# Performance work log

Hardware: AMD Instinct MI355X
Metric: run time of the kernel (lower is better)

The kernel has to match this reference:

```python
import jax, jax.numpy as jnp
import numpy as np

L, B, D, H, E, K, R = 256, 64, 1024, 16, 8, 2, 64
SCALE_ADAPTER = 0.1


def setup_inputs() -> dict:
    key = jax.random.key(0)
    ks = jax.random.split(key, 10)
    rn = lambda k, shape, s=0.02: jax.random.normal(k, shape, jnp.float32) * s
    return {
        "x": jax.random.normal(ks[0], (L, B, D), jnp.float32),
        "ln1_w": jnp.ones((D,), jnp.float32), "ln1_b": jnp.zeros((D,), jnp.float32),
        "in_proj_w": rn(ks[1], (3 * D, D)), "in_proj_b": jnp.zeros((3 * D,), jnp.float32),
        "out_proj_w": rn(ks[2], (D, D)), "out_proj_b": jnp.zeros((D,), jnp.float32),
        "ln2_w": jnp.ones((D,), jnp.float32), "ln2_b": jnp.zeros((D,), jnp.float32),
        "c_fc_w": rn(ks[3], (4 * D, D)), "c_fc_b": jnp.zeros((4 * D,), jnp.float32),
        "c_proj_w": rn(ks[4], (D, 4 * D)), "c_proj_b": jnp.zeros((D,), jnp.float32),
        "w_gate": rn(ks[5], (D, E), 0.05),
        "down_w": rn(ks[6], (E, R, D)), "down_b": jnp.zeros((E, R), jnp.float32),
        "up_w": rn(ks[7], (E, D, R)), "up_b": jnp.zeros((E, D), jnp.float32),
    }


def _layer_norm(x, w, b, eps=1e-5):
    mu = x.mean(-1, keepdims=True)
    var = ((x - mu) ** 2).mean(-1, keepdims=True)
    return (x - mu) / jnp.sqrt(var + eps) * w + b


def _mha(x, in_w, in_b, out_w, out_b):
    # x: (L,B,D) sequence-first, self-attention q=k=v=x
    hd = D // H
    qkv = x @ in_w.T + in_b                       # (L,B,3D)
    q, k, v = jnp.split(qkv, 3, axis=-1)
    q = q.reshape(L, B, H, hd)
    k = k.reshape(L, B, H, hd)
    v = v.reshape(L, B, H, hd)
    scores = jnp.einsum("lbhd,mbhd->bhlm", q, k) / jnp.sqrt(jnp.float32(hd))
    attn = jax.nn.softmax(scores, axis=-1)
    o = jnp.einsum("bhlm,mbhd->lbhd", attn, v).reshape(L, B, D)
    return o @ out_w.T + out_b


def _cv_squared(t):
    t = t.astype(jnp.float32)
    return t.var(ddof=1) / (t.mean() ** 2 + 1e-10)


def reference(x, ln1_w, ln1_b, in_proj_w, in_proj_b, out_proj_w, out_proj_b,
              ln2_w, ln2_b, c_fc_w, c_fc_b, c_proj_w, c_proj_b,
              w_gate, down_w, down_b, up_w, up_b):
    x = x + _mha(_layer_norm(x, ln1_w, ln1_b), in_proj_w, in_proj_b, out_proj_w, out_proj_b)

    # --- noisy top-k gating (eval path: no noise), routed on token 0 per sequence ---
    logits = x[0] @ w_gate                                    # (B,E)
    top_v, top_i = jax.lax.top_k(logits, min(K + 1, E))
    gk = jax.nn.softmax(top_v[:, :K], axis=1)                 # (B,K)
    gates = jnp.zeros((B, E), jnp.float32).at[jnp.arange(B)[:, None], top_i[:, :K]].set(gk)
    importance = gates.sum(0)
    load = (gates > 0).sum(0)
    moe_loss = (_cv_squared(importance) + _cv_squared(load)) * 0.01

    # --- dense dispatch/combine: y[l,b] = sum_e gates[b,e] * adapter_e(x[l,b]) ---
    h = jax.nn.relu(jnp.einsum("lbd,erd->lber", x, down_w) + down_b)     # (L,B,E,R)
    y = jnp.einsum("lber,edr,be->lbd", h, up_w, gates) + (gates @ up_b)[None]
    y = y * SCALE_ADAPTER

    # --- MLP (QuickGELU) + parallel adapter residual ---
    h2 = _layer_norm(x, ln2_w, ln2_b) @ c_fc_w.T + c_fc_b
    h2 = h2 * jax.nn.sigmoid(1.702 * h2)
    mlp = h2 @ c_proj_w.T + c_proj_b
    x = x + mlp + y
    return x, moe_loss
```

## Files before the change

kernel.cpp:

```cpp
#include <hip/hip_runtime.h>

typedef unsigned short u16;
typedef unsigned int u32;
typedef __bf16 bf16x8 __attribute__((ext_vector_type(8)));
typedef float f32x4 __attribute__((ext_vector_type(4)));

#define MFMA16(a, b, c) __builtin_amdgcn_mfma_f32_16x16x32_bf16(a, b, c, 0, 0, 0)

__device__ __forceinline__ u16 f2bf(float f) {
  u32 u = __builtin_bit_cast(u32, f);
  u32 r = u + 0x7fffu + ((u >> 16) & 1u);
  return (u16)(r >> 16);
}

__device__ __forceinline__ uint4 cvt8(const float4& a, const float4& b) {
  union { u16 h[8]; uint4 q; } u;
  u.h[0] = f2bf(a.x); u.h[1] = f2bf(a.y); u.h[2] = f2bf(a.z); u.h[3] = f2bf(a.w);
  u.h[4] = f2bf(b.x); u.h[5] = f2bf(b.y); u.h[6] = f2bf(b.z); u.h[7] = f2bf(b.w);
  return u.q;
}

__device__ __forceinline__ void gload16(const u16* g, u16* l) {
  __builtin_amdgcn_global_load_lds(
      (const __attribute__((address_space(1))) u32*)g,
      (__attribute__((address_space(3))) u32*)l, 16, 0, 0);
}

template <int MODE, int ASRC>
__global__ __launch_bounds__(256) void gemm_k(
    const void* __restrict__ Av, int lda,
    const u16* __restrict__ W, int ldb,
    const float* __restrict__ bias, const float* __restrict__ aux0,
    float* __restrict__ outF, u16* __restrict__ outB, int N, int K)
{
  __shared__ u16 As[128 * 32];
  __shared__ u16 Bs[128 * 32];
  const int tid = threadIdx.x;
  const int nxb = gridDim.x >> 7;
  const int gsz = nxb << 5;
  const int g = blockIdx.x / gsz;
  const int rem = blockIdx.x - g * gsz;
  const int m0 = ((g << 5) + (rem & 31)) * 128;
  const int n0 = (rem >> 5) * 128;
  const int w = tid >> 6, lane = tid & 63, lr = lane & 15, quad = lane >> 4;
  const int wm = (w >> 1) * 64, wn = (w & 1) * 64;

  f32x4 acc[4][4];
  #pragma unroll
  for (int i = 0; i < 4; i++)
    #pragma unroll
    for (int j = 0; j < 4; j++)
      #pragma unroll
      for (int r = 0; r < 4; r++) acc[i][j][r] = 0.f;

  const int srow = w * 32 + (lane >> 2);
  const int scol = (lane & 3) * 8;
  const u16* gB0 = W + (long)(n0 + srow) * ldb + scol;
  const u16* gB1 = gB0 + (long)16 * ldb;
  u16* lB0 = Bs + w * 1024;
  u16* lB1 = lB0 + 512;

  const u16* gA0 = nullptr; const u16* gA1 = nullptr;
  u16* lA0 = As + w * 1024; u16* lA1 = lA0 + 512;
  const float* F1 = nullptr; const float* F2 = nullptr;
  const int r0 = tid >> 2, ch0 = (tid & 3) * 8;
  if constexpr (ASRC == 0) {
    gA0 = (const u16*)Av + (long)(m0 + srow) * lda + scol;
    gA1 = gA0 + (long)16 * lda;
  } else {
    F1 = (const float*)Av + (long)(m0 + r0) * lda + ch0;
    F2 = (const float*)Av + (long)(m0 + r0 + 64) * lda + ch0;
  }

  for (int k0 = 0; k0 < K; k0 += 32) {
    if constexpr (ASRC == 0) {
      gload16(gA0 + k0, lA0);
      gload16(gA1 + k0, lA1);
      gload16(gB0 + k0, lB0);
      gload16(gB1 + k0, lB1);
      __syncthreads();
    } else {
      float4 p0 = *(const float4*)(F1 + k0);
      float4 p1 = *(const float4*)(F1 + k0 + 4);
      float4 q0 = *(const float4*)(F2 + k0);
      float4 q1 = *(const float4*)(F2 + k0 + 4);
      __syncthreads();
      gload16(gB0 + k0, lB0);
      gload16(gB1 + k0, lB1);
      *(uint4*)&As[r0 * 32 + ch0] = cvt8(p0, p1);
      *(uint4*)&As[(r0 + 64) * 32 + ch0] = cvt8(q0, q1);
      __syncthreads();
    }
    bf16x8 bfr[4];
    #pragma unroll
    for (int j = 0; j < 4; j++)
      bfr[j] = *(const bf16x8*)&Bs[(wn + j * 16 + lr) * 32 + quad * 8];
    #pragma unroll
    for (int i = 0; i < 4; i++) {
      bf16x8 af = *(const bf16x8*)&As[(wm + i * 16 + lr) * 32 + quad * 8];
      #pragma unroll
      for (int j = 0; j < 4; j++)
        acc[i][j] = MFMA16(af, bfr[j], acc[i][j]);
    }
    __syncthreads();
  }

  #pragma unroll
  for (int i = 0; i < 4; i++) {
    #pragma unroll
    for (int j = 0; j < 4; j++) {
      #pragma unroll
      for (int r = 0; r < 4; r++) {
        const int gm = m0 + wm + i * 16 + quad * 4 + r;
        const int gn = n0 + wn + j * 16 + lr;
        const long oidx = (long)gm * N + gn;
        float v = acc[i][j][r];
        if constexpr (MODE == 0) {
          v += bias[gn];
          outB[oidx] = f2bf(v);
        } else if constexpr (MODE == 1) {
          v += bias[gn] + aux0[oidx];
          outF[oidx] = v;
        } else if constexpr (MODE == 2) {
          v += bias[gn];
          v = fmaxf(v, 0.f);
          float g2 = aux0[(gm & 63) * 8 + (gn >> 6)];
          outB[oidx] = f2bf(v * g2);
        } else if constexpr (MODE == 3) {
          outF[oidx] += 0.1f * (v + aux0[(gm & 63) * 1024 + gn]);
        } else if constexpr (MODE == 4) {
          v += bias[gn];
          float e = __expf(-1.702f * v);
          v = v * __builtin_amdgcn_rcpf(1.f + e);
          outB[oidx] = f2bf(v);
        } else {
          if (bias) v += bias[gn];
          outF[oidx] += v;
        }
      }
    }
  }
}

__global__ __launch_bounds__(256) void attn_k(u16* __restrict__ qkv)
{
  __shared__ u16 Vt[64 * 264];
  __shared__ u16 Ps[32 * 264];
  __shared__ float rowstat[64];
  float* red = (float*)Ps;
  const int bh = blockIdx.x, b = bh >> 4, h = bh & 15;
  const int tid = threadIdx.x, w = tid >> 6, lane = tid & 63;
  const int lr = lane & 15, quad = lane >> 4;
  const long base = (long)b * 3072 + h * 64;

  for (int c = tid; c < 2048; c += 256) {
    int m = c >> 3, ch = (c & 7) * 8;
    uint4 vv = *(const uint4*)(qkv + (long)m * 196608 + base + 2048 + ch);
    const u16* s = (const u16*)&vv;
    #pragma unroll
    for (int t = 0; t < 8; t++) Vt[(ch + t) * 264 + m] = s[t];
  }
  __syncthreads();

  for (int qb = 0; qb < 4; qb++) {
    f32x4 acc[4][4];
    #pragma unroll
    for (int i = 0; i < 4; i++)
      #pragma unroll
      for (int j = 0; j < 4; j++)
        #pragma unroll
        for (int r = 0; r < 4; r++) acc[i][j][r] = 0.f;

    #pragma unroll
    for (int ks = 0; ks < 2; ks++) {
      bf16x8 bfr[4];
      #pragma unroll
      for (int j = 0; j < 4; j++) {
        int key = w * 64 + j * 16 + lr;
        bfr[j] = *(const bf16x8*)(qkv + (long)key * 196608 + base + 1024 + ks * 32 + quad * 8);
      }
      #pragma unroll
      for (int i = 0; i < 4; i++) {
        int gq = qb * 64 + i * 16 + lr;
        bf16x8 af = *(const bf16x8*)(qkv + (long)gq * 196608 + base + ks * 32 + quad * 8);
        #pragma unroll
        for (int j = 0; j < 4; j++)
          acc[i][j] = MFMA16(af, bfr[j], acc[i][j]);
      }
    }

    #pragma unroll
    for (int i = 0; i < 4; i++) {
      #pragma unroll
      for (int r = 0; r < 4; r++) {
        float m = -1e30f;
        #pragma unroll
        for (int j = 0; j < 4; j++) {
          float s = acc[i][j][r] * 0.125f;
          acc[i][j][r] = s;
          m = fmaxf(m, s);
        }
        #pragma unroll
        for (int off = 1; off < 16; off <<= 1) m = fmaxf(m, __shfl_xor(m, off));
        if (lr == 0) red[w * 64 + i * 16 + quad * 4 + r] = m;
      }
    }
    __syncthreads();
    if (tid < 64)
      rowstat[tid] = fmaxf(fmaxf(red[tid], red[64 + tid]),
                           fmaxf(red[128 + tid], red[192 + tid]));
    __syncthreads();

    #pragma unroll
    for (int i = 0; i < 4; i++) {
      #pragma unroll
      for (int r = 0; r < 4; r++) {
        float rm = rowstat[i * 16 + quad * 4 + r];
        float s = 0.f;
        #pragma unroll
        for (int j = 0; j < 4; j++) {
          float e = __expf(acc[i][j][r] - rm);
          acc[i][j][r] = e;
          s += e;
        }
        #pragma unroll
        for (int off = 1; off < 16; off <<= 1) s += __shfl_xor(s, off);
        if (lr == 0) red[w * 64 + i * 16 + quad * 4 + r] = s;
      }
    }
    __syncthreads();
    if (tid < 64)
      rowstat[tid] = red[tid] + red[64 + tid] + red[128 + tid] + red[192 + tid];
    __syncthreads();

    #pragma unroll
    for (int hf = 0; hf < 2; hf++) {
      #pragma unroll
      for (int ii = 0; ii < 2; ii++) {
        int i = hf * 2 + ii;
        #pragma unroll
        for (int r = 0; r < 4; r++) {
          int row = i * 16 + quad * 4 + r;
          float inv = 1.f / rowstat[row];
          #pragma unroll
          for (int j = 0; j < 4; j++)
            Ps[(row - hf * 32) * 264 + w * 64 + j * 16 + lr] =
                f2bf(acc[i][j][r] * inv);
        }
      }
      __syncthreads();
      f32x4 o[2];
      #pragma unroll
      for (int j2 = 0; j2 < 2; j2++)
        #pragma unroll
        for (int r = 0; r < 4; r++) o[j2][r] = 0.f;
      #pragma unroll
      for (int ks = 0; ks < 8; ks++) {
        bf16x8 af = *(const bf16x8*)&Ps[((w >> 1) * 16 + lr) * 264 + ks * 32 + quad * 8];
        #pragma unroll
        for (int j2 = 0; j2 < 2; j2++) {
          int j = (w & 1) * 2 + j2;
          bf16x8 bv = *(const bf16x8*)&Vt[(j * 16 + lr) * 264 + ks * 32 + quad * 8];
          o[j2] = MFMA16(af, bv, o[j2]);
        }
      }
      int l0 = qb * 64 + hf * 32 + (w >> 1) * 16 + quad * 4;
      #pragma unroll
      for (int j2 = 0; j2 < 2; j2++) {
        int j = (w & 1) * 2 + j2;
        #pragma unroll
        for (int r = 0; r < 4; r++)
          qkv[(long)(l0 + r) * 196608 + base + j * 16 + lr] = f2bf(o[j2][r]);
      }
      __syncthreads();
    }
  }
}

__global__ __launch_bounds__(256) void ln_k(const float* __restrict__ x,
                                            const float* __restrict__ wt,
                                            const float* __restrict__ bs,
                                            u16* __restrict__ out)
{
  const int tok = blockIdx.x * 4 + (threadIdx.x >> 6);
  const int lane = threadIdx.x & 63;
  const float* xp = x + (long)tok * 1024;
  float4 v[4];
  float s = 0.f, s2 = 0.f;
  #pragma unroll
  for (int t = 0; t < 4; t++) {
    v[t] = *(const float4*)(xp + t * 256 + lane * 4);
    s += v[t].x + v[t].y + v[t].z + v[t].w;
    s2 += v[t].x * v[t].x + v[t].y * v[t].y + v[t].z * v[t].z + v[t].w * v[t].w;
  }
  #pragma unroll
  for (int off = 32; off >= 1; off >>= 1) {
    s += __shfl_xor(s, off);
    s2 += __shfl_xor(s2, off);
  }
  const float m = s * (1.f / 1024.f);
  const float rstd = rsqrtf(s2 * (1.f / 1024.f) - m * m + 1e-5f);
  u16* op = out + (long)tok * 1024;
  #pragma unroll
  for (int t = 0; t < 4; t++) {
    int d = t * 256 + lane * 4;
    float4 wv = *(const float4*)(wt + d);
    float4 bv = *(const float4*)(bs + d);
    union { u16 h[4]; uint2 q; } o;
    o.h[0] = f2bf((v[t].x - m) * rstd * wv.x + bv.x);
    o.h[1] = f2bf((v[t].y - m) * rstd * wv.y + bv.y);
    o.h[2] = f2bf((v[t].z - m) * rstd * wv.z + bv.z);
    o.h[3] = f2bf((v[t].w - m) * rstd * wv.w + bv.w);
    *(uint2*)(op + d) = o.q;
  }
}

__global__ void cvtk(const float* __restrict__ src, u16* __restrict__ dst, int n4)
{
  int i = blockIdx.x * 256 + threadIdx.x;
  if (i >= n4) return;
  float4 v = ((const float4*)src)[i];
  union { u16 h[4]; uint2 q; } o;
  o.h[0] = f2bf(v.x); o.h[1] = f2bf(v.y); o.h[2] = f2bf(v.z); o.h[3] = f2bf(v.w);
  ((uint2*)dst)[i] = o.q;
}

__global__ void wupk(const float* __restrict__ up_w, u16* __restrict__ dst)
{
  int i = blockIdx.x * 256 + threadIdx.x;
  int r = i & 63, e = (i >> 6) & 7, d = i >> 9;
  dst[i] = f2bf(up_w[(e * 1024 + d) * 64 + r]);
}

__global__ __launch_bounds__(256) void gate_k(const float* __restrict__ x1,
                                              const float* __restrict__ wg,
                                              float* __restrict__ gates)
{
  const int wv = threadIdx.x >> 6, lane = threadIdx.x & 63;
  const int b = blockIdx.x * 4 + wv;
  const float* xp = x1 + (long)b * 1024;
  float lg[8];
  #pragma unroll
  for (int e = 0; e < 8; e++) lg[e] = 0.f;
  for (int i = 0; i < 16; i++) {
    int d = i * 64 + lane;
    float xv = xp[d];
    #pragma unroll
    for (int e = 0; e < 8; e++) lg[e] += xv * wg[d * 8 + e];
  }
  #pragma unroll
  for (int e = 0; e < 8; e++)
    #pragma unroll
    for (int off = 32; off >= 1; off >>= 1) lg[e] += __shfl_xor(lg[e], off);
  if (lane == 0) {
    int e1 = 0; float v1 = lg[0];
    #pragma unroll
    for (int e = 1; e < 8; e++) if (lg[e] > v1) { v1 = lg[e]; e1 = e; }
    int e2 = -1; float v2 = -1e30f;
    #pragma unroll
    for (int e = 0; e < 8; e++) if (e != e1 && lg[e] > v2) { v2 = lg[e]; e2 = e; }
    float ex = __expf(v2 - v1);
    float inv = 1.f / (1.f + ex);
    #pragma unroll
    for (int e = 0; e < 8; e++)
      gates[b * 8 + e] = (e == e1) ? inv : ((e == e2) ? ex * inv : 0.f);
  }
}

__global__ void moe_loss_k(const float* __restrict__ gates, float* __restrict__ out)
{
  if (threadIdx.x != 0) return;
  float imp[8], ld[8];
  for (int e = 0; e < 8; e++) { imp[e] = 0.f; ld[e] = 0.f; }
  for (int b = 0; b < 64; b++)
    for (int e = 0; e < 8; e++) {
      float g = gates[b * 8 + e];
      imp[e] += g;
      if (g > 0.f) ld[e] += 1.f;
    }
  float mi = 0.f, ml = 0.f;
  for (int e = 0; e < 8; e++) { mi += imp[e]; ml += ld[e]; }
  mi *= 0.125f; ml *= 0.125f;
  float vi = 0.f, vl = 0.f;
  for (int e = 0; e < 8; e++) {
    float a = imp[e] - mi; vi += a * a;
    float c = ld[e] - ml; vl += c * c;
  }
  vi *= (1.f / 7.f); vl *= (1.f / 7.f);
  out[0] = 0.01f * (vi / (mi * mi + 1e-10f) + vl / (ml * ml + 1e-10f));
}

__global__ __launch_bounds__(256) void gb_k(const float* __restrict__ gates,
                                            const float* __restrict__ up_b,
                                            float* __restrict__ gb)
{
  int b = blockIdx.x, d0 = threadIdx.x * 4;
  float g[8];
  #pragma unroll
  for (int e = 0; e < 8; e++) g[e] = gates[b * 8 + e];
  float s0 = 0, s1 = 0, s2 = 0, s3 = 0;
  #pragma unroll
  for (int e = 0; e < 8; e++) {
    float4 u = *(const float4*)(up_b + e * 1024 + d0);
    s0 += g[e] * u.x; s1 += g[e] * u.y; s2 += g[e] * u.z; s3 += g[e] * u.w;
  }
  float4 r; r.x = s0; r.y = s1; r.z = s2; r.w = s3;
  *(float4*)(gb + b * 1024 + d0) = r;
}

extern "C" void kernel_launch(void* const* d_in, const int* in_sizes, int n_in,
                              void* d_out, int out_size, void* d_ws, size_t ws_size,
                              hipStream_t stream)
{
  (void)in_sizes; (void)n_in; (void)out_size;
  const float* x      = (const float*)d_in[0];
  const float* ln1_w  = (const float*)d_in[1];
  const float* ln1_b  = (const float*)d_in[2];
  const float* in_w   = (const float*)d_in[3];
  const float* in_b   = (const float*)d_in[4];
  const float* out_w  = (const float*)d_in[5];
  const float* out_b  = (const float*)d_in[6];
  const float* ln2_w  = (const float*)d_in[7];
  const float* ln2_b  = (const float*)d_in[8];
  const float* fc_w   = (const float*)d_in[9];
  const float* fc_b   = (const float*)d_in[10];
  const float* pj_w   = (const float*)d_in[11];
  const float* pj_b   = (const float*)d_in[12];
  const float* w_gate = (const float*)d_in[13];
  const float* down_w = (const float*)d_in[14];
  const float* down_b = (const float*)d_in[15];
  const float* up_w   = (const float*)d_in[16];
  const float* up_b   = (const float*)d_in[17];
  float* out = (float*)d_out;
  char* ws = (char*)d_ws;

  u16* wb_in   = (u16*)(ws + 0);
  u16* wb_out  = (u16*)(ws + 6291456);
  u16* wb_down = (u16*)(ws + 8388608);
  u16* wb_up   = (u16*)(ws + 9437184);
  u16* wb_fc   = (u16*)(ws + 0);
  u16* wb_pj   = (u16*)(ws + 10485760);
  float* gates = (float*)(ws + 19005440);
  float* gb    = (float*)(ws + 19007488);
  u16* qkv     = (u16*)(ws + 19269632);
  u16* xln2    = (u16*)(ws + 19269632);
  u16* hg      = (u16*)(ws + 52824064);
  u16* h2      = (u16*)(ws + 69601280);
  u16* xln = (u16*)d_out;

  const bool big = ws_size >= (size_t)203819008;

  cvtk<<<3072, 256, 0, stream>>>(in_w, wb_in, 786432);
  cvtk<<<1024, 256, 0, stream>>>(out_w, wb_out, 262144);
  cvtk<<<512, 256, 0, stream>>>(down_w, wb_down, 131072);
  wupk<<<2048, 256, 0, stream>>>(up_w, wb_up);

  ln_k<<<4096, 256, 0, stream>>>(x, ln1_w, ln1_b, xln);
  gemm_k<0, 0><<<24 * 128, 256, 0, stream>>>(
      xln, 1024, wb_in, 1024, in_b, nullptr, nullptr, qkv, 3072, 1024);

  attn_k<<<1024, 256, 0, stream>>>(qkv);

  gemm_k<1, 0><<<8 * 128, 256, 0, stream>>>(
      qkv, 3072, wb_out, 1024, out_b, x, out, nullptr, 1024, 1024);

  gate_k<<<16, 256, 0, stream>>>(out, w_gate, gates);
  moe_loss_k<<<1, 64, 0, stream>>>(gates, out + 16777216);
  gb_k<<<64, 256, 0, stream>>>(gates, up_b, gb);

  ln_k<<<4096, 256, 0, stream>>>(out, ln2_w, ln2_b, xln2);

  gemm_k<2, 2><<<4 * 128, 256, 0, stream>>>(
      out, 1024, wb_down, 1024, down_b, gates, nullptr, hg, 512, 1024);
  gemm_k<3, 0><<<8 * 128, 256, 0, stream>>>(
      hg, 512, wb_up, 512, nullptr, gb, out, nullptr, 1024, 512);

  cvtk<<<4096, 256, 0, stream>>>(fc_w, wb_fc, 1048576);
  cvtk<<<4096, 256, 0, stream>>>(pj_w, wb_pj, 1048576);

  if (big) {
    gemm_k<4, 0><<<32 * 128, 256, 0, stream>>>(
        xln2, 1024, wb_fc, 1024, fc_b, nullptr, nullptr, h2, 4096, 1024);
    gemm_k<5, 0><<<8 * 128, 256, 0, stream>>>(
        h2, 4096, wb_pj, 4096, pj_b, nullptr, out, nullptr, 1024, 4096);
  } else {
    for (int c = 0; c < 4; c++) {
      gemm_k<4, 0><<<8 * 128, 256, 0, stream>>>(
          xln2, 1024, wb_fc + (long)c * 1048576, 1024, fc_b + c * 1024,
          nullptr, nullptr, h2, 1024, 1024);
      gemm_k<5, 0><<<8 * 128, 256, 0, stream>>>(
          h2, 1024, wb_pj + c * 1024, 4096, (c == 0) ? pj_b : nullptr,
          nullptr, out, nullptr, 1024, 1024);
    }
  }
}
```

Baseline: 1.082 ms.

## Double-buffer GEMM shared-memory tiles to overlap global loads with MFMA

Splits the A and B LDS tiles into two buffers. The kernel prefetches the next K-slice into the idle buffer while MFMAs consume the current one, which drops one barrier per iteration. For fp32 A inputs, the next slice is loaded into registers before the MFMAs and converted and stored to LDS after them. This doubles LDS use per block, which may lower occupancy, and adds register pressure from the held prefetch values. The fp32 store path is guarded only for ASRC==2, so any other non-zero ASRC would never write its A tile.

```diff
diff --git a/kernel.cpp b/kernel.cpp
--- a/kernel.cpp
+++ b/kernel.cpp
@@ -33,8 +33,8 @@
     const float* __restrict__ bias, const float* __restrict__ aux0,
     float* __restrict__ outF, u16* __restrict__ outB, int N, int K)
 {
-  __shared__ u16 As[128 * 32];
-  __shared__ u16 Bs[128 * 32];
+  __shared__ u16 As[2][128 * 32];
+  __shared__ u16 Bs[2][128 * 32];
   const int tid = threadIdx.x;
   const int nxb = gridDim.x >> 7;
   const int gsz = nxb << 5;
@@ -57,11 +57,9 @@
   const int scol = (lane & 3) * 8;
   const u16* gB0 = W + (long)(n0 + srow) * ldb + scol;
   const u16* gB1 = gB0 + (long)16 * ldb;
-  u16* lB0 = Bs + w * 1024;
-  u16* lB1 = lB0 + 512;
+  const int lo = w * 1024;
 
   const u16* gA0 = nullptr; const u16* gA1 = nullptr;
-  u16* lA0 = As + w * 1024; u16* lA1 = lA0 + 512;
   const float* F1 = nullptr; const float* F2 = nullptr;
   const int r0 = tid >> 2, ch0 = (tid & 3) * 8;
   if constexpr (ASRC == 0) {
@@ -72,37 +70,71 @@
     F2 = (const float*)Av + (long)(m0 + r0 + 64) * lda + ch0;
   }
 
+  int cur = 0;
+
+  if constexpr (ASRC == 0) {
+    gload16(gA0, &As[0][lo]);
+    gload16(gA1, &As[0][lo + 512]);
+    gload16(gB0, &Bs[0][lo]);
+    gload16(gB1, &Bs[0][lo + 512]);
+  } else {
+    float4 p0 = *(const float4*)(F1);
+    float4 p1 = *(const float4*)(F1 + 4);
+    float4 q0 = *(const float4*)(F2);
+    float4 q1 = *(const float4*)(F2 + 4);
+    gload16(gB0, &Bs[0][lo]);
+    gload16(gB1, &Bs[0][lo + 512]);
+    *(uint4*)&As[0][r0 * 32 + ch0] = cvt8(p0, p1);
+    *(uint4*)&As[0][(r0 + 64) * 32 + ch0] = cvt8(q0, q1);
+  }
+  __syncthreads();
+
   for (int k0 = 0; k0 < K; k0 += 32) {
+    const int kn = k0 + 32;
+    const bool more = kn < K;
+
+    float4 p0, p1, q0, q1;
     if constexpr (ASRC == 0) {
-      gload16(gA0 + k0, lA0);
-      gload16(gA1 + k0, lA1);
-      gload16(gB0 + k0, lB0);
-      gload16(gB1 + k0, lB1);
-      __syncthreads();
+      if (more) {
+        gload16(gA0 + kn, &As[cur ^ 1][lo]);
+        gload16(gA1 + kn, &As[cur ^ 1][lo + 512]);
+        gload16(gB0 + kn, &Bs[cur ^ 1][lo]);
+        gload16(gB1 + kn, &Bs[cur ^ 1][lo + 512]);
+      }
     } else {
-      float4 p0 = *(const float4*)(F1 + k0);
-      float4 p1 = *(const float4*)(F1 + k0 + 4);
-      float4 q0 = *(const float4*)(F2 + k0);
-      float4 q1 = *(const float4*)(F2 + k0 + 4);
-      __syncthreads();
-      gload16(gB0 + k0, lB0);
-      gload16(gB1 + k0, lB1);
-      *(uint4*)&As[r0 * 32 + ch0] = cvt8(p0, p1);
-      *(uint4*)&As[(r0 + 64) * 32 + ch0] = cvt8(q0, q1);
-      __syncthreads();
-    }
+      if (more) {
+        p0 = *(const float4*)(F1 + kn);
+        p1 = *(const float4*)(F1 + kn + 4);
+        q0 = *(const float4*)(F2 + kn);
+        q1 = *(const float4*)(F2 + kn + 4);
+        gload16(gB0 + kn, &Bs[cur ^ 1][lo]);
+        gload16(gB1 + kn, &Bs[cur ^ 1][lo + 512]);
+      }
+    }
+
+    const u16* Asc = As[cur];
+    const u16* Bsc = Bs[cur];
     bf16x8 bfr[4];
     #pragma unroll
     for (int j = 0; j < 4; j++)
-      bfr[j] = *(const bf16x8*)&Bs[(wn + j * 16 + lr) * 32 + quad * 8];
+      bfr[j] = *(const bf16x8*)&Bsc[(wn + j * 16 + lr) * 32 + quad * 8];
     #pragma unroll
     for (int i = 0; i < 4; i++) {
-      bf16x8 af = *(const bf16x8*)&As[(wm + i * 16 + lr) * 32 + quad * 8];
+      bf16x8 af = *(const bf16x8*)&Asc[(wm + i * 16 + lr) * 32 + quad * 8];
       #pragma unroll
       for (int j = 0; j < 4; j++)
         acc[i][j] = MFMA16(af, bfr[j], acc[i][j]);
     }
+
+    if constexpr (ASRC == 2) {
+      if (more) {
+        *(uint4*)&As[cur ^ 1][r0 * 32 + ch0] = cvt8(p0, p1);
+        *(uint4*)&As[cur ^ 1][(r0 + 64) * 32 + ch0] = cvt8(q0, q1);
+      }
+    }
+
     __syncthreads();
+    cur ^= 1;
   }
 
   #pragma unroll
```

Result: faster. 1.053 ms (-2.7%).
